# Performance work log

Measured on AMD Instinct MI355X. Metric: run time of the kernel, lower is better.

## Reference

```python
import jax, jax.numpy as jnp
import numpy as np

B, L, D, H = 2, 1024, 1024, 16
HD = D // H  # head_dim = 64
EPS = 1e-12  # F.normalize default eps


def setup_inputs() -> dict:
    key = jax.random.key(0)
    ks = jax.random.split(key, 7)
    s = 1.0 / np.sqrt(D)
    return {
        "x": jax.random.normal(ks[0], (B, L, D), dtype=jnp.float32),
        "Wq": jax.random.normal(ks[1], (D, D), dtype=jnp.float32) * s,
        "Wk": jax.random.normal(ks[2], (D, D), dtype=jnp.float32) * s,
        "Wv": jax.random.normal(ks[3], (D, D), dtype=jnp.float32) * s,
        "Wo": jax.random.normal(ks[4], (D, D), dtype=jnp.float32) * s,
        "Wb": jax.random.normal(ks[5], (D, H), dtype=jnp.float32) * s,
        "bb": jnp.zeros((H,), dtype=jnp.float32),
    }


def _l2norm(t):
    # matches F.normalize(t, dim=-1): t / max(||t||_2, eps)
    n = jnp.sqrt(jnp.sum(t * t, axis=-1, keepdims=True))
    return t / jnp.maximum(n, EPS)


def reference(x, Wq, Wk, Wv, Wo, Wb, bb):
    q = (x @ Wq).reshape(B, L, H, HD)
    k = (x @ Wk).reshape(B, L, H, HD)
    v = (x @ Wv).reshape(B, L, H, HD)
    beta = jax.nn.sigmoid(x @ Wb + bb)          # [B, L, H]
    q = _l2norm(q)
    k = _l2norm(k)
    # gated outer products: [B, L, H, HD, HD]
    kv = jnp.einsum('blhd,blhe->blhde', k, v) * beta[..., None, None]
    kv_cumsum = jnp.cumsum(kv, axis=1)          # causal cumulative kv state
    out = jnp.einsum('blhd,blhde->blhe', q, kv_cumsum)  # [B, L, H, HD]
    return out.reshape(B, L, D) @ Wo
```

## Files before the change

### kernel.cpp

```cpp
#include <hip/hip_runtime.h>
#include <math.h>

#define BB   2
#define LL   1024
#define DD   1024
#define HH   16
#define HDIM 64
#define MM   (BB * LL)
#define CHK  64
#define NCHK (LL / CHK)

typedef short bf16x8 __attribute__((ext_vector_type(8)));
typedef float f32x4  __attribute__((ext_vector_type(4)));
typedef const __attribute__((address_space(1))) unsigned int* gas_ptr;
typedef __attribute__((address_space(3))) unsigned int* las_ptr;

__device__ __forceinline__ void gload16(const void* g, void* l) {
    __builtin_amdgcn_global_load_lds((gas_ptr)(unsigned long long)g,
                                     (las_ptr)(unsigned long long)l, 16, 0, 0);
}

__device__ __forceinline__ unsigned short f2bf(float f) {
    unsigned int u = __float_as_uint(f);
    u += 0x7fffu + ((u >> 16) & 1u);
    return (unsigned short)(u >> 16);
}
__device__ __forceinline__ float bfhi(unsigned int u) { return __uint_as_float(u & 0xffff0000u); }
__device__ __forceinline__ float bflo(unsigned int u) { return __uint_as_float(u << 16); }

__device__ __forceinline__ bf16x8 frag70(const unsigned short* a, int row, int tc) {
    const unsigned int* p = (const unsigned int*)(a + row * 70 + tc);
    union { unsigned int u[4]; bf16x8 v; } r;
    r.u[0] = p[0]; r.u[1] = p[1]; r.u[2] = p[2]; r.u[3] = p[3];
    return r.v;
}

__global__ void prep_all(const float* __restrict__ x, unsigned short* __restrict__ xb,
                         const float* __restrict__ Wb, unsigned short* __restrict__ Wbt,
                         const float* __restrict__ W0, const float* __restrict__ W1,
                         const float* __restrict__ W2, const float* __restrict__ W3,
                         unsigned short* __restrict__ T0, unsigned short* __restrict__ T1,
                         unsigned short* __restrict__ T2, unsigned short* __restrict__ T3) {
    const int bid = blockIdx.x;
    if (bid < 2048) {
        const int idx = bid * 256 + threadIdx.x;
        const float4 v = ((const float4*)x)[idx];
        ushort4 o;
        o.x = f2bf(v.x); o.y = f2bf(v.y); o.z = f2bf(v.z); o.w = f2bf(v.w);
        ((ushort4*)xb)[idx] = o;
        return;
    }
    if (bid < 2112) {
        const int t = (bid - 2048) * 256 + threadIdx.x;
        const int h = t >> 10, kidx = t & 1023;
        Wbt[t] = f2bf(Wb[kidx * HH + h]);
        return;
    }
    __shared__ float tile[32][33];
    const int b4 = bid - 2112;
    const int which = b4 >> 10;
    const int b = b4 & 1023;
    const int bk = b >> 5, bn = b & 31;
    const float* W = which == 0 ? W0 : which == 1 ? W1 : which == 2 ? W2 : W3;
    unsigned short* T = which == 0 ? T0 : which == 1 ? T1 : which == 2 ? T2 : T3;
    const int tx = threadIdx.x & 31, ty = threadIdx.x >> 5;
#pragma unroll
    for (int i = 0; i < 4; ++i)
        tile[ty + i * 8][tx] = W[(size_t)(bk * 32 + ty + i * 8) * DD + bn * 32 + tx];
    __syncthreads();
#pragma unroll
    for (int i = 0; i < 4; ++i)
        T[(size_t)(bn * 32 + ty + i * 8) * DD + bk * 32 + tx] = f2bf(tile[tx][ty + i * 8]);
}

__device__ __forceinline__ void gemm_kloop(const unsigned short* A, const unsigned short* Bt,
                                           unsigned short* As, unsigned short* Bs,
                                           int rowBase, int colBase, int K,
                                           f32x4 acc[4][4]) {
    const int tid = threadIdx.x;
    const int c0 = tid, c1 = tid + 256;
    const int ar0 = c0 >> 2, ak0 = (c0 & 3) << 3;
    const int ar1 = c1 >> 2, ak1 = (c1 & 3) << 3;
    const unsigned short* Ag0 = A + (size_t)(rowBase + ar0) * K + ak0;
    const unsigned short* Ag1 = A + (size_t)(rowBase + ar1) * K + ak1;
    const unsigned short* Bg0 = Bt + (size_t)(colBase + ar0) * K + ak0;
    const unsigned short* Bg1 = Bt + (size_t)(colBase + ar1) * K + ak1;
    unsigned short* Al0 = As + c0 * 8; unsigned short* Al1 = As + c1 * 8;
    unsigned short* Bl0 = Bs + c0 * 8; unsigned short* Bl1 = Bs + c1 * 8;
    const int lane = tid & 63, wv = tid >> 6;
    const int qr = wv >> 1, qc = wv & 1;
    const int fr = lane & 15;
    const int koff = (lane >> 4) << 3;
    int aoff[4], boff[4];
#pragma unroll
    for (int mi = 0; mi < 4; ++mi) aoff[mi] = (qr * 64 + mi * 16 + fr) * 32 + koff;
#pragma unroll
    for (int nj = 0; nj < 4; ++nj) boff[nj] = (qc * 64 + nj * 16 + fr) * 32 + koff;

    for (int k0 = 0; k0 < K; k0 += 32) {
        __syncthreads();
        gload16(Ag0, Al0); gload16(Ag1, Al1);
        gload16(Bg0, Bl0); gload16(Bg1, Bl1);
        Ag0 += 32; Ag1 += 32; Bg0 += 32; Bg1 += 32;
        __syncthreads();
        bf16x8 av[4], bv[4];
#pragma unroll
        for (int mi = 0; mi < 4; ++mi) av[mi] = *(const bf16x8*)(As + aoff[mi]);
#pragma unroll
        for (int nj = 0; nj < 4; ++nj) bv[nj] = *(const bf16x8*)(Bs + boff[nj]);
#pragma unroll
        for (int mi = 0; mi < 4; ++mi)
#pragma unroll
            for (int nj = 0; nj < 4; ++nj)
                acc[mi][nj] = __builtin_amdgcn_mfma_f32_16x16x32_bf16(av[mi], bv[nj], acc[mi][nj], 0, 0, 0);
    }
}

__global__ __launch_bounds__(256) void gemm_qkv_beta(const unsigned short* __restrict__ xb,
                                                     const unsigned short* __restrict__ Wqt,
                                                     const unsigned short* __restrict__ Wkt,
                                                     const unsigned short* __restrict__ Wvt,
                                                     const unsigned short* __restrict__ Wbt,
                                                     const float* __restrict__ bbp,
                                                     unsigned short* __restrict__ qb,
                                                     unsigned short* __restrict__ kb,
                                                     unsigned short* __restrict__ vb,
                                                     float* __restrict__ beta) {
    __shared__ unsigned short As[128 * 32];
    __shared__ unsigned short Bs[128 * 32];
    const int lane = threadIdx.x & 63, wv = threadIdx.x >> 6;
    const int fr = lane & 15, quad = lane >> 4;
    if (blockIdx.x >= 384) {
        const int rowBase = (blockIdx.x - 384) * 128;
        const int r0 = rowBase + wv * 32 + fr;
        f32x4 bacc[2];
        bacc[0] = (f32x4){0.f, 0.f, 0.f, 0.f};
        bacc[1] = (f32x4){0.f, 0.f, 0.f, 0.f};
        for (int k0 = 0; k0 < DD; k0 += 32) {
            const int kk = k0 + quad * 8;
            const bf16x8 a0 = *(const bf16x8*)&xb[(size_t)r0 * DD + kk];
            const bf16x8 a1 = *(const bf16x8*)&xb[(size_t)(r0 + 16) * DD + kk];
            const bf16x8 bw = *(const bf16x8*)&Wbt[(size_t)fr * DD + kk];
            bacc[0] = __builtin_amdgcn_mfma_f32_16x16x32_bf16(a0, bw, bacc[0], 0, 0, 0);
            bacc[1] = __builtin_amdgcn_mfma_f32_16x16x32_bf16(a1, bw, bacc[1], 0, 0, 0);
        }
        const float bias = bbp[fr];
#pragma unroll
        for (int mi = 0; mi < 2; ++mi)
#pragma unroll
            for (int i = 0; i < 4; ++i) {
                const int row = rowBase + wv * 32 + mi * 16 + quad * 4 + i;
                const float s = bacc[mi][i] + bias;
                beta[row * HH + fr] = 1.0f / (1.0f + expf(-s));
            }
        return;
    }
    const int by = blockIdx.x / 24, bxx = blockIdx.x % 24;
    const int mat = bxx >> 3, tn = bxx & 7;
    const unsigned short* Bt = mat == 0 ? Wqt : (mat == 1 ? Wkt : Wvt);
    unsigned short* Cout = mat == 0 ? qb : (mat == 1 ? kb : vb);
    f32x4 acc[4][4];
#pragma unroll
    for (int mi = 0; mi < 4; ++mi)
#pragma unroll
        for (int nj = 0; nj < 4; ++nj) acc[mi][nj] = (f32x4){0.f, 0.f, 0.f, 0.f};
    gemm_kloop(xb, Bt, As, Bs, by * 128, tn * 128, DD, acc);

    const int qr = wv >> 1, qc = wv & 1;
    if (mat < 2) {
#pragma unroll
        for (int mi = 0; mi < 4; ++mi)
#pragma unroll
            for (int i = 0; i < 4; ++i) {
                float s = 0.f;
#pragma unroll
                for (int nj = 0; nj < 4; ++nj) { float t = acc[mi][nj][i]; s += t * t; }
                s += __shfl_xor(s, 1, 64);
                s += __shfl_xor(s, 2, 64);
                s += __shfl_xor(s, 4, 64);
                s += __shfl_xor(s, 8, 64);
                const float inv = 1.0f / fmaxf(sqrtf(s), 1e-12f);
#pragma unroll
                for (int nj = 0; nj < 4; ++nj) acc[mi][nj][i] *= inv;
            }
    }
#pragma unroll
    for (int mi = 0; mi < 4; ++mi)
#pragma unroll
        for (int i = 0; i < 4; ++i) {
            const int row = by * 128 + qr * 64 + mi * 16 + quad * 4 + i;
#pragma unroll
            for (int nj = 0; nj < 4; ++nj) {
                const int col = tn * 128 + qc * 64 + nj * 16 + fr;
                Cout[(size_t)row * DD + col] = f2bf(acc[mi][nj][i]);
            }
        }
}

__global__ __launch_bounds__(256) void chunkkv_kernel(const unsigned short* __restrict__ k,
                                                      const unsigned short* __restrict__ v,
                                                      const float* __restrict__ beta,
                                                      float* __restrict__ states) {
    const int c = blockIdx.x % NCHK;
    const int bh = blockIdx.x / NCHK;
    const int b = bh / HH, h = bh % HH;
    __shared__ unsigned short kT[64 * 70];
    __shared__ unsigned short vT[64 * 70];
    const int tid = threadIdx.x;
    for (int i = tid; i < 512; i += 256) {
        const int t = i >> 3, dg = (i & 7) << 3;
        const int m = b * LL + c * CHK + t;
        const float be = beta[m * HH + h];
        const size_t go = (size_t)m * DD + h * 64 + dg;
        const uint4 ku = *(const uint4*)&k[go];
        const uint4 vu = *(const uint4*)&v[go];
        unsigned int kw[4] = {ku.x, ku.y, ku.z, ku.w};
        unsigned int vw[4] = {vu.x, vu.y, vu.z, vu.w};
#pragma unroll
        for (int jj = 0; jj < 4; ++jj) {
            kT[(dg + 2 * jj)     * 70 + t] = f2bf(bflo(kw[jj]) * be);
            kT[(dg + 2 * jj + 1) * 70 + t] = f2bf(bfhi(kw[jj]) * be);
            vT[(dg + 2 * jj)     * 70 + t] = (unsigned short)(vw[jj] & 0xffffu);
            vT[(dg + 2 * jj + 1) * 70 + t] = (unsigned short)(vw[jj] >> 16);
        }
    }
    __syncthreads();
    const int lane = tid & 63, wv = tid >> 6;
    const int fr = lane & 15, quad = lane >> 4;
    f32x4 acc[4];
#pragma unroll
    for (int et = 0; et < 4; ++et) acc[et] = (f32x4){0.f, 0.f, 0.f, 0.f};
#pragma unroll
    for (int kh = 0; kh < 2; ++kh) {
        const int tc = kh * 32 + quad * 8;
        const bf16x8 a = frag70(kT, wv * 16 + fr, tc);
#pragma unroll
        for (int et = 0; et < 4; ++et) {
            const bf16x8 bb = frag70(vT, et * 16 + fr, tc);
            acc[et] = __builtin_amdgcn_mfma_f32_16x16x32_bf16(a, bb, acc[et], 0, 0, 0);
        }
    }
    float* outp = states + ((size_t)bh * NCHK + c) * 4096;
#pragma unroll
    for (int et = 0; et < 4; ++et)
#pragma unroll
        for (int i = 0; i < 4; ++i) {
            const int d = wv * 16 + quad * 4 + i;
            const int e = et * 16 + fr;
            outp[d * 64 + e] = acc[et][i];
        }
}

__global__ __launch_bounds__(256) void attn_kernel(const unsigned short* __restrict__ q,
                                                   const unsigned short* __restrict__ k,
                                                   const unsigned short* __restrict__ v,
                                                   const float* __restrict__ beta,
                                                   const float* __restrict__ states,
                                                   unsigned short* __restrict__ y) {
    const int c = blockIdx.x % NCHK;
    const int bh = blockIdx.x / NCHK;
    const int b = bh / HH, h = bh % HH;
    __shared__ unsigned short qS[64 * 80];
    __shared__ unsigned short kS[64 * 80];
    __shared__ unsigned short sS[64 * 80];
    __shared__ unsigned short vT[64 * 70];
    __shared__ unsigned short sT[64 * 70];
    const int tid = threadIdx.x;
    for (int i = tid; i < 512; i += 256) {
        const int t = i >> 3, dg = (i & 7) << 3;
        const int m = b * LL + c * CHK + t;
        const float be = beta[m * HH + h];
        const size_t go = (size_t)m * DD + h * 64 + dg;
        const uint4 qu = *(const uint4*)&q[go];
        const uint4 ku = *(const uint4*)&k[go];
        const uint4 vu = *(const uint4*)&v[go];
        *(uint4*)&qS[t * 80 + dg] = qu;
        *(uint4*)&kS[t * 80 + dg] = ku;
        unsigned int vw[4] = {vu.x, vu.y, vu.z, vu.w};
#pragma unroll
        for (int jj = 0; jj < 4; ++jj) {
            vT[(dg + 2 * jj)     * 70 + t] = f2bf(bflo(vw[jj]) * be);
            vT[(dg + 2 * jj + 1) * 70 + t] = f2bf(bfhi(vw[jj]) * be);
        }
    }
    {
        float racc[16];
#pragma unroll
        for (int j = 0; j < 16; ++j) racc[j] = 0.f;
        const float* sbase = states + (size_t)bh * NCHK * 4096;
        for (int cc = 0; cc < c; ++cc) {
            const float* sp = sbase + cc * 4096;
#pragma unroll
            for (int j = 0; j < 16; ++j) racc[j] += sp[j * 256 + tid];
        }
        const int e = tid & 63;
        const int dbase = tid >> 6;
#pragma unroll
        for (int j = 0; j < 16; ++j)
            sT[e * 70 + j * 4 + dbase] = f2bf(racc[j]);
    }
    __syncthreads();
    const int lane = tid & 63, wv = tid >> 6;
    const int fr = lane & 15, quad = lane >> 4;
    const int koff = quad * 8;
    f32x4 s_acc[4];
#pragma unroll
    for (int j = 0; j < 4; ++j) s_acc[j] = (f32x4){0.f, 0.f, 0.f, 0.f};
#pragma unroll
    for (int kh = 0; kh < 2; ++kh) {
        const bf16x8 a = *(const bf16x8*)&qS[(wv * 16 + fr) * 80 + kh * 32 + koff];
#pragma unroll
        for (int j = 0; j < 4; ++j) {
            const bf16x8 bb = *(const bf16x8*)&kS[(j * 16 + fr) * 80 + kh * 32 + koff];
            s_acc[j] = __builtin_amdgcn_mfma_f32_16x16x32_bf16(a, bb, s_acc[j], 0, 0, 0);
        }
    }
#pragma unroll
    for (int j = 0; j < 4; ++j)
#pragma unroll
        for (int i = 0; i < 4; ++i) {
            const int t = wv * 16 + quad * 4 + i;
            const int s = j * 16 + fr;
            sS[t * 80 + s] = (s <= t) ? f2bf(s_acc[j][i]) : (unsigned short)0;
        }
    f32x4 o_acc[4];
#pragma unroll
    for (int j = 0; j < 4; ++j) o_acc[j] = (f32x4){0.f, 0.f, 0.f, 0.f};
#pragma unroll
    for (int kh = 0; kh < 2; ++kh) {
        const bf16x8 a = *(const bf16x8*)&sS[(wv * 16 + fr) * 80 + kh * 32 + koff];
#pragma unroll
        for (int j = 0; j < 4; ++j) {
            const bf16x8 bb = frag70(vT, j * 16 + fr, kh * 32 + koff);
            o_acc[j] = __builtin_amdgcn_mfma_f32_16x16x32_bf16(a, bb, o_acc[j], 0, 0, 0);
        }
    }
#pragma unroll
    for (int kh = 0; kh < 2; ++kh) {
        const bf16x8 a = *(const bf16x8*)&qS[(wv * 16 + fr) * 80 + kh * 32 + koff];
#pragma unroll
        for (int j = 0; j < 4; ++j) {
            const bf16x8 bb = frag70(sT, j * 16 + fr, kh * 32 + koff);
            o_acc[j] = __builtin_amdgcn_mfma_f32_16x16x32_bf16(a, bb, o_acc[j], 0, 0, 0);
        }
    }
#pragma unroll
    for (int j = 0; j < 4; ++j)
#pragma unroll
        for (int i = 0; i < 4; ++i) {
            const int m = b * LL + c * CHK + wv * 16 + quad * 4 + i;
            const int e = j * 16 + fr;
            y[(size_t)m * DD + h * 64 + e] = f2bf(o_acc[j][i]);
        }
}

__global__ __launch_bounds__(256) void gemm_out(const unsigned short* __restrict__ yb,
                                                const unsigned short* __restrict__ Wot,
                                                float* __restrict__ out) {
    __shared__ unsigned short As[64 * 32];
    __shared__ unsigned short Bs[128 * 32];
    const int by = blockIdx.x >> 3, tn = blockIdx.x & 7;
    const int tid = threadIdx.x;
    const int rowBase = by * 64, colBase = tn * 128;
    const int ar = tid >> 2, ak = (tid & 3) << 3;
    const unsigned short* Ag = yb + (size_t)(rowBase + ar) * DD + ak;
    unsigned short* Al = As + tid * 8;
    const int c1 = tid + 256;
    const int br1 = c1 >> 2, bk1 = (c1 & 3) << 3;
    const unsigned short* Bg0 = Wot + (size_t)(colBase + ar) * DD + ak;
    const unsigned short* Bg1 = Wot + (size_t)(colBase + br1) * DD + bk1;
    unsigned short* Bl0 = Bs + tid * 8; unsigned short* Bl1 = Bs + c1 * 8;
    const int lane = tid & 63, wv = tid >> 6;
    const int rh = wv & 1, ch = wv >> 1;
    const int fr = lane & 15, koff = (lane >> 4) << 3;
    int aoff[2], boff[4];
#pragma unroll
    for (int mi = 0; mi < 2; ++mi) aoff[mi] = (rh * 32 + mi * 16 + fr) * 32 + koff;
#pragma unroll
    for (int nj = 0; nj < 4; ++nj) boff[nj] = (ch * 64 + nj * 16 + fr) * 32 + koff;
    f32x4 acc[2][4];
#pragma unroll
    for (int mi = 0; mi < 2; ++mi)
#pragma unroll
        for (int nj = 0; nj < 4; ++nj) acc[mi][nj] = (f32x4){0.f, 0.f, 0.f, 0.f};
    for (int k0 = 0; k0 < DD; k0 += 32) {
        __syncthreads();
        gload16(Ag, Al); gload16(Bg0, Bl0); gload16(Bg1, Bl1);
        Ag += 32; Bg0 += 32; Bg1 += 32;
        __syncthreads();
        bf16x8 av[2], bv[4];
#pragma unroll
        for (int mi = 0; mi < 2; ++mi) av[mi] = *(const bf16x8*)(As + aoff[mi]);
#pragma unroll
        for (int nj = 0; nj < 4; ++nj) bv[nj] = *(const bf16x8*)(Bs + boff[nj]);
#pragma unroll
        for (int mi = 0; mi < 2; ++mi)
#pragma unroll
            for (int nj = 0; nj < 4; ++nj)
                acc[mi][nj] = __builtin_amdgcn_mfma_f32_16x16x32_bf16(av[mi], bv[nj], acc[mi][nj], 0, 0, 0);
    }
    const int quad = lane >> 4;
#pragma unroll
    for (int mi = 0; mi < 2; ++mi)
#pragma unroll
        for (int i = 0; i < 4; ++i) {
            const int row = rowBase + rh * 32 + mi * 16 + quad * 4 + i;
#pragma unroll
            for (int nj = 0; nj < 4; ++nj) {
                const int col = colBase + ch * 64 + nj * 16 + fr;
                out[(size_t)row * DD + col] = acc[mi][nj][i];
            }
        }
}

extern "C" void kernel_launch(void* const* d_in, const int* in_sizes, int n_in,
                              void* d_out, int out_size, void* d_ws, size_t ws_size,
                              hipStream_t stream) {
    (void)in_sizes; (void)n_in; (void)out_size; (void)ws_size;
    const float* x  = (const float*)d_in[0];
    const float* Wq = (const float*)d_in[1];
    const float* Wk = (const float*)d_in[2];
    const float* Wv = (const float*)d_in[3];
    const float* Wo = (const float*)d_in[4];
    const float* Wb = (const float*)d_in[5];
    const float* bbp = (const float*)d_in[6];
    float* out = (float*)d_out;

    char* ws = (char*)d_ws;
    unsigned short* xb  = (unsigned short*)ws;                      ws += (size_t)MM * DD * 2;
    unsigned short* Wqt = (unsigned short*)ws;                      ws += (size_t)DD * DD * 2;
    unsigned short* Wkt = (unsigned short*)ws;                      ws += (size_t)DD * DD * 2;
    unsigned short* Wvt = (unsigned short*)ws;                      ws += (size_t)DD * DD * 2;
    unsigned short* Wot = (unsigned short*)ws;                      ws += (size_t)DD * DD * 2;
    unsigned short* Wbt = (unsigned short*)ws;                      ws += (size_t)HH * DD * 2;
    unsigned short* qb  = (unsigned short*)ws;                      ws += (size_t)MM * DD * 2;
    unsigned short* kb  = (unsigned short*)ws;                      ws += (size_t)MM * DD * 2;
    unsigned short* vb  = (unsigned short*)ws;                      ws += (size_t)MM * DD * 2;
    unsigned short* yb  = (unsigned short*)ws;                      ws += (size_t)MM * DD * 2;
    float*          beta   = (float*)ws;                            ws += (size_t)MM * HH * 4;
    float*          states = (float*)ws;                            ws += (size_t)BB * HH * NCHK * 4096 * 4;

    prep_all<<<6208, 256, 0, stream>>>(x, xb, Wb, Wbt, Wq, Wk, Wv, Wo, Wqt, Wkt, Wvt, Wot);
    gemm_qkv_beta<<<400, 256, 0, stream>>>(xb, Wqt, Wkt, Wvt, Wbt, bbp, qb, kb, vb, beta);
    chunkkv_kernel<<<BB * HH * NCHK, 256, 0, stream>>>(kb, vb, beta, states);
    attn_kernel<<<BB * HH * NCHK, 256, 0, stream>>>(qb, kb, vb, beta, states, yb);
    gemm_out<<<32 * 8, 256, 0, stream>>>(yb, Wot, out);
}
```

Measured before the change: 145.9 us.

## Double-buffer GEMM LDS tiles and store chunk states in bf16

Both projection GEMMs now use two LDS buffers: the next K-slice is fetched with global_load_lds while MFMAs run on the current one, so each iteration needs one barrier instead of two. The per-chunk KV states are written as bf16 in a transposed, coalesced layout through an LDS staging tile, and read back with vector loads. This halves state traffic and simplifies the prefix sum. LDS tiles change from a 70 to a 72 stride so fragments can be read as aligned 16-byte vectors. The trade-offs are double the GEMM LDS footprint, which may lower occupancy, and extra rounding from storing states in bf16.

New measurement: 134.4 us (median of 2 runs). -7.9%, faster.

```diff
diff --git a/kernel.cpp b/kernel.cpp
--- a/kernel.cpp
+++ b/kernel.cpp
@@ -27,13 +27,6 @@
 }
 __device__ __forceinline__ float bfhi(unsigned int u) { return __uint_as_float(u & 0xffff0000u); }
 __device__ __forceinline__ float bflo(unsigned int u) { return __uint_as_float(u << 16); }
-
-__device__ __forceinline__ bf16x8 frag70(const unsigned short* a, int row, int tc) {
-    const unsigned int* p = (const unsigned int*)(a + row * 70 + tc);
-    union { unsigned int u[4]; bf16x8 v; } r;
-    r.u[0] = p[0]; r.u[1] = p[1]; r.u[2] = p[2]; r.u[3] = p[3];
-    return r.v;
-}
 
 __global__ void prep_all(const float* __restrict__ x, unsigned short* __restrict__ xb,
                          const float* __restrict__ Wb, unsigned short* __restrict__ Wbt,
@@ -73,10 +66,10 @@
         T[(size_t)(bn * 32 + ty + i * 8) * DD + bk * 32 + tx] = f2bf(tile[tx][ty + i * 8]);
 }
 
-__device__ __forceinline__ void gemm_kloop(const unsigned short* A, const unsigned short* Bt,
-                                           unsigned short* As, unsigned short* Bs,
-                                           int rowBase, int colBase, int K,
-                                           f32x4 acc[4][4]) {
+__device__ __forceinline__ void gemm_kloop_db(const unsigned short* A, const unsigned short* Bt,
+                                              unsigned short* As, unsigned short* Bs,
+                                              int rowBase, int colBase, int K,
+                                              f32x4 acc[4][4]) {
     const int tid = threadIdx.x;
     const int c0 = tid, c1 = tid + 256;
     const int ar0 = c0 >> 2, ak0 = (c0 & 3) << 3;
@@ -85,8 +78,6 @@
     const unsigned short* Ag1 = A + (size_t)(rowBase + ar1) * K + ak1;
     const unsigned short* Bg0 = Bt + (size_t)(colBase + ar0) * K + ak0;
     const unsigned short* Bg1 = Bt + (size_t)(colBase + ar1) * K + ak1;
-    unsigned short* Al0 = As + c0 * 8; unsigned short* Al1 = As + c1 * 8;
-    unsigned short* Bl0 = Bs + c0 * 8; unsigned short* Bl1 = Bs + c1 * 8;
     const int lane = tid & 63, wv = tid >> 6;
     const int qr = wv >> 1, qc = wv & 1;
     const int fr = lane & 15;
@@ -97,17 +88,26 @@
 #pragma unroll
     for (int nj = 0; nj < 4; ++nj) boff[nj] = (qc * 64 + nj * 16 + fr) * 32 + koff;
 
+    gload16(Ag0, As + c0 * 8); gload16(Ag1, As + c1 * 8);
+    gload16(Bg0, Bs + c0 * 8); gload16(Bg1, Bs + c1 * 8);
+    Ag0 += 32; Ag1 += 32; Bg0 += 32; Bg1 += 32;
+
     for (int k0 = 0; k0 < K; k0 += 32) {
+        const int cur = (k0 >> 5) & 1;
+        const int nxt = cur ^ 1;
         __syncthreads();
-        gload16(Ag0, Al0); gload16(Ag1, Al1);
-        gload16(Bg0, Bl0); gload16(Bg1, Bl1);
-        Ag0 += 32; Ag1 += 32; Bg0 += 32; Bg1 += 32;
-        __syncthreads();
+        if (k0 + 32 < K) {
+            gload16(Ag0, As + nxt * 4096 + c0 * 8); gload16(Ag1, As + nxt * 4096 + c1 * 8);
+            gload16(Bg0, Bs + nxt * 4096 + c0 * 8); gload16(Bg1, Bs + nxt * 4096 + c1 * 8);
+            Ag0 += 32; Ag1 += 32; Bg0 += 32; Bg1 += 32;
+        }
+        const unsigned short* Ab = As + cur * 4096;
+        const unsigned short* Bb = Bs + cur * 4096;
         bf16x8 av[4], bv[4];
 #pragma unroll
-        for (int mi = 0; mi < 4; ++mi) av[mi] = *(const bf16x8*)(As + aoff[mi]);
-#pragma unroll
-        for (int nj = 0; nj < 4; ++nj) bv[nj] = *(const bf16x8*)(Bs + boff[nj]);
+        for (int mi = 0; mi < 4; ++mi) av[mi] = *(const bf16x8*)(Ab + aoff[mi]);
+#pragma unroll
+        for (int nj = 0; nj < 4; ++nj) bv[nj] = *(const bf16x8*)(Bb + boff[nj]);
 #pragma unroll
         for (int mi = 0; mi < 4; ++mi)
 #pragma unroll
@@ -126,8 +126,8 @@
                                                      unsigned short* __restrict__ kb,
                                                      unsigned short* __restrict__ vb,
                                                      float* __restrict__ beta) {
-    __shared__ unsigned short As[128 * 32];
-    __shared__ unsigned short Bs[128 * 32];
+    __shared__ unsigned short As[2 * 128 * 32];
+    __shared__ unsigned short Bs[2 * 128 * 32];
     const int lane = threadIdx.x & 63, wv = threadIdx.x >> 6;
     const int fr = lane & 15, quad = lane >> 4;
     if (blockIdx.x >= 384) {
@@ -164,7 +164,7 @@
     for (int mi = 0; mi < 4; ++mi)
 #pragma unroll
         for (int nj = 0; nj < 4; ++nj) acc[mi][nj] = (f32x4){0.f, 0.f, 0.f, 0.f};
-    gemm_kloop(xb, Bt, As, Bs, by * 128, tn * 128, DD, acc);
+    gemm_kloop_db(xb, Bt, As, Bs, by * 128, tn * 128, DD, acc);
 
     const int qr = wv >> 1, qc = wv & 1;
     if (mat < 2) {
@@ -200,12 +200,13 @@
 __global__ __launch_bounds__(256) void chunkkv_kernel(const unsigned short* __restrict__ k,
                                                       const unsigned short* __restrict__ v,
                                                       const float* __restrict__ beta,
-                                                      float* __restrict__ states) {
+                                                      unsigned short* __restrict__ states) {
     const int c = blockIdx.x % NCHK;
     const int bh = blockIdx.x / NCHK;
     const int b = bh / HH, h = bh % HH;
-    __shared__ unsigned short kT[64 * 70];
-    __shared__ unsigned short vT[64 * 70];
+    __shared__ __align__(16) unsigned short kT[64 * 72];
+    __shared__ __align__(16) unsigned short vT[64 * 72];
+    __shared__ __align__(16) unsigned short tT[64 * 72];
     const int tid = threadIdx.x;
     for (int i = tid; i < 512; i += 256) {
         const int t = i >> 3, dg = (i & 7) << 3;
@@ -218,10 +219,10 @@
         unsigned int vw[4] = {vu.x, vu.y, vu.z, vu.w};
 #pragma unroll
         for (int jj = 0; jj < 4; ++jj) {
-            kT[(dg + 2 * jj)     * 70 + t] = f2bf(bflo(kw[jj]) * be);
-            kT[(dg + 2 * jj + 1) * 70 + t] = f2bf(bfhi(kw[jj]) * be);
-            vT[(dg + 2 * jj)     * 70 + t] = (unsigned short)(vw[jj] & 0xffffu);
-            vT[(dg + 2 * jj + 1) * 70 + t] = (unsigned short)(vw[jj] >> 16);
+            kT[(dg + 2 * jj)     * 72 + t] = f2bf(bflo(kw[jj]) * be);
+            kT[(dg + 2 * jj + 1) * 72 + t] = f2bf(bfhi(kw[jj]) * be);
+            vT[(dg + 2 * jj)     * 72 + t] = (unsigned short)(vw[jj] & 0xffffu);
+            vT[(dg + 2 * jj + 1) * 72 + t] = (unsigned short)(vw[jj] >> 16);
         }
     }
     __syncthreads();
@@ -233,38 +234,42 @@
 #pragma unroll
     for (int kh = 0; kh < 2; ++kh) {
         const int tc = kh * 32 + quad * 8;
-        const bf16x8 a = frag70(kT, wv * 16 + fr, tc);
+        const bf16x8 a = *(const bf16x8*)&kT[(wv * 16 + fr) * 72 + tc];
 #pragma unroll
         for (int et = 0; et < 4; ++et) {
-            const bf16x8 bb = frag70(vT, et * 16 + fr, tc);
+            const bf16x8 bb = *(const bf16x8*)&vT[(et * 16 + fr) * 72 + tc];
             acc[et] = __builtin_amdgcn_mfma_f32_16x16x32_bf16(a, bb, acc[et], 0, 0, 0);
         }
     }
-    float* outp = states + ((size_t)bh * NCHK + c) * 4096;
 #pragma unroll
     for (int et = 0; et < 4; ++et)
 #pragma unroll
-        for (int i = 0; i < 4; ++i) {
-            const int d = wv * 16 + quad * 4 + i;
-            const int e = et * 16 + fr;
-            outp[d * 64 + e] = acc[et][i];
-        }
+        for (int i = 0; i < 4; ++i)
+            tT[(et * 16 + fr) * 72 + wv * 16 + quad * 4 + i] = f2bf(acc[et][i]);
+    __syncthreads();
+    unsigned short* outp = states + ((size_t)bh * NCHK + c) * 4096;
+#pragma unroll
+    for (int s = 0; s < 2; ++s) {
+        const int p = tid * 16 + s * 8;
+        const int e = p >> 6, d = p & 63;
+        *(uint4*)&outp[p] = *(const uint4*)&tT[e * 72 + d];
+    }
 }
 
 __global__ __launch_bounds__(256) void attn_kernel(const unsigned short* __restrict__ q,
                                                    const unsigned short* __restrict__ k,
                                                    const unsigned short* __restrict__ v,
                                                    const float* __restrict__ beta,
-                                                   const float* __restrict__ states,
+                                                   const unsigned short* __restrict__ states,
                                                    unsigned short* __restrict__ y) {
     const int c = blockIdx.x % NCHK;
     const int bh = blockIdx.x / NCHK;
     const int b = bh / HH, h = bh % HH;
-    __shared__ unsigned short qS[64 * 80];
-    __shared__ unsigned short kS[64 * 80];
-    __shared__ unsigned short sS[64 * 80];
-    __shared__ unsigned short vT[64 * 70];
-    __shared__ unsigned short sT[64 * 70];
+    __shared__ __align__(16) unsigned short qS[64 * 80];
+    __shared__ __align__(16) unsigned short kS[64 * 80];
+    __shared__ __align__(16) unsigned short sS[64 * 80];
+    __shared__ __align__(16) unsigned short vT[64 * 72];
+    __shared__ __align__(16) unsigned short sT[64 * 72];
     const int tid = threadIdx.x;
     for (int i = tid; i < 512; i += 256) {
         const int t = i >> 3, dg = (i & 7) << 3;
@@ -279,25 +284,30 @@
         unsigned int vw[4] = {vu.x, vu.y, vu.z, vu.w};
 #pragma unroll
         for (int jj = 0; jj < 4; ++jj) {
-            vT[(dg + 2 * jj)     * 70 + t] = f2bf(bflo(vw[jj]) * be);
-            vT[(dg + 2 * jj + 1) * 70 + t] = f2bf(bfhi(vw[jj]) * be);
+            vT[(dg + 2 * jj)     * 72 + t] = f2bf(bflo(vw[jj]) * be);
+            vT[(dg + 2 * jj + 1) * 72 + t] = f2bf(bfhi(vw[jj]) * be);
         }
     }
     {
         float racc[16];
 #pragma unroll
         for (int j = 0; j < 16; ++j) racc[j] = 0.f;
-        const float* sbase = states + (size_t)bh * NCHK * 4096;
+        const unsigned short* sbase = states + (size_t)bh * NCHK * 4096;
+        const int p0 = tid * 16;
         for (int cc = 0; cc < c; ++cc) {
-            const float* sp = sbase + cc * 4096;
-#pragma unroll
-            for (int j = 0; j < 16; ++j) racc[j] += sp[j * 256 + tid];
-        }
-        const int e = tid & 63;
-        const int dbase = tid >> 6;
+            const uint4 u0 = *(const uint4*)&sbase[cc * 4096 + p0];
+            const uint4 u1 = *(const uint4*)&sbase[cc * 4096 + p0 + 8];
+            const unsigned int w[8] = {u0.x, u0.y, u0.z, u0.w, u1.x, u1.y, u1.z, u1.w};
+#pragma unroll
+            for (int j = 0; j < 8; ++j) {
+                racc[2 * j]     += bflo(w[j]);
+                racc[2 * j + 1] += bfhi(w[j]);
+            }
+        }
+        const int e = p0 >> 6, d0 = p0 & 63;
 #pragma unroll
         for (int j = 0; j < 16; ++j)
-            sT[e * 70 + j * 4 + dbase] = f2bf(racc[j]);
+            sT[e * 72 + d0 + j] = f2bf(racc[j]);
     }
     __syncthreads();
     const int lane = tid & 63, wv = tid >> 6;
@@ -331,7 +341,7 @@
         const bf16x8 a = *(const bf16x8*)&sS[(wv * 16 + fr) * 80 + kh * 32 + koff];
 #pragma unroll
         for (int j = 0; j < 4; ++j) {
-            const bf16x8 bb = frag70(vT, j * 16 + fr, kh * 32 + koff);
+            const bf16x8 bb = *(const bf16x8*)&vT[(j * 16 + fr) * 72 + kh * 32 + koff];
             o_acc[j] = __builtin_amdgcn_mfma_f32_16x16x32_bf16(a, bb, o_acc[j], 0, 0, 0);
         }
     }
@@ -340,7 +350,7 @@
         const bf16x8 a = *(const bf16x8*)&qS[(wv * 16 + fr) * 80 + kh * 32 + koff];
 #pragma unroll
         for (int j = 0; j < 4; ++j) {
-            const bf16x8 bb = frag70(sT, j * 16 + fr, kh * 32 + koff);
+            const bf16x8 bb = *(const bf16x8*)&sT[(j * 16 + fr) * 72 + kh * 32 + koff];
             o_acc[j] = __builtin_amdgcn_mfma_f32_16x16x32_bf16(a, bb, o_acc[j], 0, 0, 0);
         }
     }
@@ -357,19 +367,17 @@
 __global__ __launch_bounds__(256) void gemm_out(const unsigned short* __restrict__ yb,
                                                 const unsigned short* __restrict__ Wot,
                                                 float* __restrict__ out) {
-    __shared__ unsigned short As[64 * 32];
-    __shared__ unsigned short Bs[128 * 32];
+    __shared__ unsigned short As[2 * 64 * 32];
+    __shared__ unsigned short Bs[2 * 128 * 32];
     const int by = blockIdx.x >> 3, tn = blockIdx.x & 7;
     const int tid = threadIdx.x;
     const int rowBase = by * 64, colBase = tn * 128;
     const int ar = tid >> 2, ak = (tid & 3) << 3;
     const unsigned short* Ag = yb + (size_t)(rowBase + ar) * DD + ak;
-    unsigned short* Al = As + tid * 8;
     const int c1 = tid + 256;
     const int br1 = c1 >> 2, bk1 = (c1 & 3) << 3;
     const unsigned short* Bg0 = Wot + (size_t)(colBase + ar) * DD + ak;
     const unsigned short* Bg1 = Wot + (size_t)(colBase + br1) * DD + bk1;
-    unsigned short* Bl0 = Bs + tid * 8; unsigned short* Bl1 = Bs + c1 * 8;
     const int lane = tid & 63, wv = tid >> 6;
     const int rh = wv & 1, ch = wv >> 1;
     const int fr = lane & 15, koff = (lane >> 4) << 3;
@@ -383,16 +391,27 @@
     for (int mi = 0; mi < 2; ++mi)
 #pragma unroll
         for (int nj = 0; nj < 4; ++nj) acc[mi][nj] = (f32x4){0.f, 0.f, 0.f, 0.f};
+
+    gload16(Ag, As + tid * 8);
+    gload16(Bg0, Bs + tid * 8); gload16(Bg1, Bs + c1 * 8);
+    Ag += 32; Bg0 += 32; Bg1 += 32;
+
     for (int k0 = 0; k0 < DD; k0 += 32) {
+        const int cur = (k0 >> 5) & 1;
+        const int nxt = cur ^ 1;
         __syncthreads();
-        gload16(Ag, Al); gload16(Bg0, Bl0); gload16(Bg1, Bl1);
-        Ag += 32; Bg0 += 32; Bg1 += 32;
-        __syncthreads();
+        if (k0 + 32 < DD) {
+            gload16(Ag, As + nxt * 2048 + tid * 8);
+            gload16(Bg0, Bs + nxt * 4096 + tid * 8); gload16(Bg1, Bs + nxt * 4096 + c1 * 8);
+            Ag += 32; Bg0 += 32; Bg1 += 32;
+        }
+        const unsigned short* Ab = As + cur * 2048;
+        const unsigned short* Bb = Bs + cur * 4096;
         bf16x8 av[2], bv[4];
 #pragma unroll
-        for (int mi = 0; mi < 2; ++mi) av[mi] = *(const bf16x8*)(As + aoff[mi]);
-#pragma unroll
-        for (int nj = 0; nj < 4; ++nj) bv[nj] = *(const bf16x8*)(Bs + boff[nj]);
+        for (int mi = 0; mi < 2; ++mi) av[mi] = *(const bf16x8*)(Ab + aoff[mi]);
+#pragma unroll
+        for (int nj = 0; nj < 4; ++nj) bv[nj] = *(const bf16x8*)(Bb + boff[nj]);
 #pragma unroll
         for (int mi = 0; mi < 2; ++mi)
 #pragma unroll
@@ -438,7 +457,7 @@
     unsigned short* vb  = (unsigned short*)ws;                      ws += (size_t)MM * DD * 2;
     unsigned short* yb  = (unsigned short*)ws;                      ws += (size_t)MM * DD * 2;
     float*          beta   = (float*)ws;                            ws += (size_t)MM * HH * 4;
-    float*          states = (float*)ws;                            ws += (size_t)BB * HH * NCHK * 4096 * 4;
+    unsigned short* states = (unsigned short*)ws;                   ws += (size_t)BB * HH * NCHK * 4096 * 2;
 
     prep_all<<<6208, 256, 0, stream>>>(x, xb, Wb, Wbt, Wq, Wk, Wv, Wo, Wqt, Wkt, Wvt, Wot);
     gemm_qkv_beta<<<400, 256, 0, stream>>>(xb, Wqt, Wkt, Wvt, Wbt, bbp, qb, kb, vb, beta);
```
